# Optimization experiments

Measured on AMD Instinct MI355X. Metric: run time of the kernel, lower is better.

## Reference

```python
import jax, jax.numpy as jnp
import numpy as np

ATTEN_SIZE = 16
HIDDEN = 512


def setup_inputs() -> dict:
    key = jax.random.key(0)
    ks = jax.random.split(key, 6)
    B, S, D_in, H, D_out = 64, 100, 256, HIDDEN, 256
    # xavier-normal-ish scale for weights
    def xav(k, shape):
        fan_in, fan_out = shape
        std = np.sqrt(2.0 / (fan_in + fan_out))
        return jax.random.normal(k, shape, dtype=jnp.float32) * std
    return {
        "x": jax.random.normal(ks[0], (B, S, D_in), dtype=jnp.float32),
        "W0": xav(ks[1], (D_in, H)),
        "b0": jnp.zeros((1, 1, H), dtype=jnp.float32),
        "Wq": xav(ks[2], (H, H)),
        "Wk": xav(ks[3], (H, H)),
        "Wv": xav(ks[4], (H, H)),
        "W1": xav(ks[5], (H, D_out)),
        "b1": jnp.zeros((1, 1, D_out), dtype=jnp.float32),
    }


def reference(x, W0, b0, Wq, Wk, Wv, W1, b1):
    w = ATTEN_SIZE
    win = 2 * w + 1
    B, S = x.shape[0], x.shape[1]
    # pre-attention MLP layer (atten_layer_index = 1)
    h = jax.nn.relu(x @ W0 + b0)  # [B, S, H]
    # sliding-window neighbor gather, matching pad + roll(k) + stack + slice:
    # x_nei[:, i, k_idx] = padded[:, i + 2w - k_idx]  (reversed window order)
    padded = jnp.pad(h, ((0, 0), (w, w), (0, 0)))  # [B, S+2w, H]
    idx = jnp.arange(S)[:, None] + (2 * w - jnp.arange(win))[None, :]
    x_nei = padded[:, idx]
    q = x_nei @ Wq
    k = x_nei @ Wk
    v = x_nei @ Wv
    d = jnp.einsum('bswh,buh_->bswu'.replace('h_', 'sh'[1] + 'h'), q, k) if False else jnp.einsum('bswh,bsuh->bswu', q, k)
    d = d / jnp.sqrt(jnp.float32(HIDDEN))
    alpha = jax.nn.softmax(d, axis=-1)
    wv = jnp.einsum('bswu,bsuh->bswh', alpha, v)
    out = wv.sum(axis=2)  # sum over window rows -> [B, S, H]
    y = jax.nn.relu(out @ W1 + b1)  # [B, S, D_out]
    return y, alpha.reshape(B * S, win, win)
```

## Files before the change

### kernel.cpp

```cpp
#include <hip/hip_runtime.h>

typedef __bf16 bf16x8 __attribute__((ext_vector_type(8)));
typedef float f32x4 __attribute__((ext_vector_type(4)));

__device__ __forceinline__ unsigned short f2bf(float f) {
  unsigned int u = __float_as_uint(f);
  u += 0x7FFFu + ((u >> 16) & 1u);
  return (unsigned short)(u >> 16);
}
__device__ __forceinline__ float bf2f(unsigned short s) {
  return __uint_as_float(((unsigned int)s) << 16);
}

__global__ __launch_bounds__(256) void prep_kernel(
    const float* __restrict__ x, const float* __restrict__ W0,
    const float* __restrict__ Wq, const float* __restrict__ Wk,
    const float* __restrict__ Wv, const float* __restrict__ W1,
    unsigned short* __restrict__ xb, unsigned short* __restrict__ w0t,
    unsigned short* __restrict__ wqkvt, unsigned short* __restrict__ w1t)
{
  int idx = blockIdx.x * 256 + threadIdx.x;
  const int XB = 6400 * 256, W0T = 512 * 256, WQKV = 1536 * 512, W1T = 256 * 512;
  if (idx < XB) { xb[idx] = f2bf(x[idx]); return; }
  idx -= XB;
  if (idx < W0T) {
    int n = idx >> 8, k = idx & 255;
    w0t[idx] = f2bf(W0[k * 512 + n]); return;
  }
  idx -= W0T;
  if (idx < WQKV) {
    int n = idx >> 9, k = idx & 511;
    float v = (n < 512) ? Wq[k * 512 + n]
            : (n < 1024) ? Wk[k * 512 + (n - 512)]
                         : Wv[k * 512 + (n - 1024)];
    wqkvt[idx] = f2bf(v); return;
  }
  idx -= WQKV;
  if (idx < W1T) {
    int n = idx >> 9, k = idx & 511;
    w1t[idx] = f2bf(W1[k * 256 + n]);
  }
}

template<bool RELU, bool OUT_BF16>
__global__ __launch_bounds__(64) void gemm_mfma(
    const unsigned short* __restrict__ A, int lda,
    const unsigned short* __restrict__ Bt, int ldb,
    const float* __restrict__ bias,
    void* __restrict__ Cout, int ldc, int K)
{
  const int m0 = blockIdx.x * 64;
  const int n0 = blockIdx.y * 64;
  const int l  = threadIdx.x;
  const int lr = l & 15;
  const int kq = l >> 4;
  f32x4 acc[4][4];
#pragma unroll
  for (int i = 0; i < 4; i++)
#pragma unroll
    for (int j = 0; j < 4; j++) acc[i][j] = (f32x4){0.f, 0.f, 0.f, 0.f};

  const unsigned short* Ap = A  + (long)(m0 + lr) * lda + 8 * kq;
  const unsigned short* Bp = Bt + (long)(n0 + lr) * ldb + 8 * kq;

  for (int k0 = 0; k0 < K; k0 += 32) {
    bf16x8 af[4], bfr[4];
#pragma unroll
    for (int i = 0; i < 4; i++)
      af[i] = *(const bf16x8*)(Ap + (long)(16 * i) * lda + k0);
#pragma unroll
    for (int j = 0; j < 4; j++)
      bfr[j] = *(const bf16x8*)(Bp + (long)(16 * j) * ldb + k0);
#pragma unroll
    for (int i = 0; i < 4; i++)
#pragma unroll
      for (int j = 0; j < 4; j++)
        acc[i][j] = __builtin_amdgcn_mfma_f32_16x16x32_bf16(af[i], bfr[j], acc[i][j], 0, 0, 0);
  }

#pragma unroll
  for (int i = 0; i < 4; i++) {
#pragma unroll
    for (int j = 0; j < 4; j++) {
      int col = n0 + 16 * j + lr;
      float bv = bias ? bias[col] : 0.0f;
#pragma unroll
      for (int r = 0; r < 4; r++) {
        int row = m0 + 16 * i + 4 * kq + r;
        float v = acc[i][j][r] + bv;
        if (RELU) v = fmaxf(v, 0.0f);
        if (OUT_BF16) ((unsigned short*)Cout)[(long)row * ldc + col] = f2bf(v);
        else          ((float*)Cout)[(long)row * ldc + col] = v;
      }
    }
  }
}

__global__ __launch_bounds__(64) void gram_kernel(
    const unsigned short* __restrict__ qkv, float* __restrict__ G)
{
  const float scale = 0.044194173824159216f;
  const int it = blockIdx.x;
  const int b  = blockIdx.y;
  const int l = threadIdx.x, lr = l & 15, kq = l >> 4;
  const unsigned short* qrow = qkv + (long)(b * 100 + it * 16 + lr) * 1536 + 8 * kq;
  const unsigned short* krow = qkv + (long)(b * 100 + lr) * 1536 + 512 + 8 * kq;
  f32x4 acc[7];
#pragma unroll
  for (int j = 0; j < 7; j++) acc[j] = (f32x4){0.f, 0.f, 0.f, 0.f};
  for (int k0 = 0; k0 < 512; k0 += 32) {
    bf16x8 aq = *(const bf16x8*)(qrow + k0);
#pragma unroll
    for (int j = 0; j < 7; j++) {
      bf16x8 bk = *(const bf16x8*)(krow + (long)(j * 16) * 1536 + k0);
      acc[j] = __builtin_amdgcn_mfma_f32_16x16x32_bf16(aq, bk, acc[j], 0, 0, 0);
    }
  }
  float* Gb = G + (long)b * 10000;
#pragma unroll
  for (int j = 0; j < 7; j++) {
#pragma unroll
    for (int r = 0; r < 4; r++) {
      int i  = it * 16 + 4 * kq + r;
      int jj = j * 16 + lr;
      if (i < 100 && jj < 100) Gb[i * 100 + jj] = acc[j][r] * scale;
    }
  }
}

__global__ __launch_bounds__(256) void attn_kernel(
    const float* __restrict__ G,
    const unsigned short* __restrict__ qkv,
    float* __restrict__ alpha_out,
    unsigned short* __restrict__ outb)
{
  const int blk = blockIdx.x;
  const int b = blk / 100, s = blk % 100;
  __shared__ float dmat[33][36];
  __shared__ float rowmax[33], rowinv[33];
  __shared__ float beta[36];
  const int tid = threadIdx.x;
  const float* Gb = G + (long)b * 10000;

  for (int t = tid; t < 1089; t += 256) {
    int dw = t / 33, du = t % 33;
    int i = s + 16 - dw, j = s + 16 - du;
    float v = 0.f;
    if ((unsigned)i < 100u && (unsigned)j < 100u) v = Gb[i * 100 + j];
    dmat[dw][du] = v;
  }
  __syncthreads();

  if (tid < 132) {
    int row = tid >> 2, g = tid & 3;
    float m = -1e30f;
    for (int u = g; u < 33; u += 4) m = fmaxf(m, dmat[row][u]);
    m = fmaxf(m, __shfl_xor(m, 1));
    m = fmaxf(m, __shfl_xor(m, 2));
    float ssum = 0.f;
    for (int u = g; u < 33; u += 4) ssum += __expf(dmat[row][u] - m);
    ssum += __shfl_xor(ssum, 1);
    ssum += __shfl_xor(ssum, 2);
    if (g == 0) { rowmax[row] = m; rowinv[row] = 1.0f / ssum; }
  }
  __syncthreads();

  float* aout = alpha_out + (long)blk * 1089;
  for (int t = tid; t < 1089; t += 256) {
    int dw = t / 33, du = t % 33;
    float a = __expf(dmat[dw][du] - rowmax[dw]) * rowinv[dw];
    aout[t] = a;
    dmat[dw][du] = a;
  }
  __syncthreads();

  if (tid < 33) {
    float sum = 0.f;
    for (int w = 0; w < 33; ++w) sum += dmat[w][tid];
    beta[tid] = sum;
  }
  __syncthreads();

  const unsigned short* vbase = qkv + (long)(b * 100) * 1536 + 1024;
  {
    int c = tid;
    float acc0 = 0.f, acc1 = 0.f;
    for (int u = 0; u < 33; ++u) {
      int p = s + 16 - u;
      if ((unsigned)p < 100u) {
        float bw = beta[u];
        const unsigned short* vr = vbase + (long)p * 1536;
        acc0 += bw * bf2f(vr[c]);
        acc1 += bw * bf2f(vr[c + 256]);
      }
    }
    unsigned short* orow = outb + (long)blk * 512;
    orow[c]       = f2bf(acc0);
    orow[c + 256] = f2bf(acc1);
  }
}

extern "C" void kernel_launch(void* const* d_in, const int* in_sizes, int n_in,
                              void* d_out, int out_size, void* d_ws, size_t ws_size,
                              hipStream_t stream) {
  const float* x  = (const float*)d_in[0];
  const float* W0 = (const float*)d_in[1];
  const float* b0 = (const float*)d_in[2];
  const float* Wq = (const float*)d_in[3];
  const float* Wk = (const float*)d_in[4];
  const float* Wv = (const float*)d_in[5];
  const float* W1 = (const float*)d_in[6];
  const float* b1 = (const float*)d_in[7];

  char* ws = (char*)d_ws;
  unsigned short* xb    = (unsigned short*)(ws + 0);
  unsigned short* w0t   = (unsigned short*)(ws + 3276800);
  unsigned short* wqkvt = (unsigned short*)(ws + 3538944);
  unsigned short* w1t   = (unsigned short*)(ws + 5111808);
  unsigned short* h     = (unsigned short*)(ws + 5373952);
  unsigned short* qkv   = (unsigned short*)(ws + 11927552);
  float*          G     = (float*)(ws + 31637504);
  unsigned short* outb  = (unsigned short*)(ws + 34197504);

  float* y_out     = (float*)d_out;
  float* alpha_out = y_out + 6400 * 256;

  prep_kernel<<<10496, 256, 0, stream>>>(x, W0, Wq, Wk, Wv, W1, xb, w0t, wqkvt, w1t);
  gemm_mfma<true,  true ><<<dim3(100, 8),  64, 0, stream>>>(xb, 256, w0t, 256, b0, h, 512, 256);
  gemm_mfma<false, true ><<<dim3(100, 24), 64, 0, stream>>>(h, 512, wqkvt, 512, nullptr, qkv, 1536, 512);
  gram_kernel<<<dim3(7, 64), 64, 0, stream>>>(qkv, G);
  attn_kernel<<<6400, 256, 0, stream>>>(G, qkv, alpha_out, outb);
  gemm_mfma<true,  false><<<dim3(100, 4), 64, 0, stream>>>(outb, 512, w1t, 512, b1, y_out, 256, 512);
}
```

Before: 211.3 us.

## Stage GEMM tiles in LDS with async double-buffered loads; tile weight transposes

Replaces the single-wave GEMM and gram kernels, which loaded operands straight from global memory, with 256-thread blocks. These stage 64x32 A and 128x32 B tiles into LDS through global_load_lds and double-buffer them, so loading the next K-slice overlaps the MFMAs on the current one and the tiles are shared across four waves. The prep kernel now converts x with float4 loads and transposes the weights through a padded shared-memory tile, so both reads and writes are coalesced. Gram now reads 128 K rows where 100 are valid, so it computes extra padded work. Workspace offsets shift to make room for that overread.

```diff
diff --git a/kernel.cpp b/kernel.cpp
--- a/kernel.cpp
+++ b/kernel.cpp
@@ -2,6 +2,7 @@
 
 typedef __bf16 bf16x8 __attribute__((ext_vector_type(8)));
 typedef float f32x4 __attribute__((ext_vector_type(4)));
+typedef unsigned int u32;
 
 __device__ __forceinline__ unsigned short f2bf(float f) {
   unsigned int u = __float_as_uint(f);
@@ -10,6 +11,12 @@
 }
 __device__ __forceinline__ float bf2f(unsigned short s) {
   return __uint_as_float(((unsigned int)s) << 16);
+}
+
+__device__ __forceinline__ void gload16(const void* g, void* l) {
+  __builtin_amdgcn_global_load_lds(
+      (const __attribute__((address_space(1))) u32*)g,
+      (__attribute__((address_space(3))) u32*)l, 16, 0, 0);
 }
 
 __global__ __launch_bounds__(256) void prep_kernel(
@@ -19,75 +26,108 @@
     unsigned short* __restrict__ xb, unsigned short* __restrict__ w0t,
     unsigned short* __restrict__ wqkvt, unsigned short* __restrict__ w1t)
 {
-  int idx = blockIdx.x * 256 + threadIdx.x;
-  const int XB = 6400 * 256, W0T = 512 * 256, WQKV = 1536 * 512, W1T = 256 * 512;
-  if (idx < XB) { xb[idx] = f2bf(x[idx]); return; }
-  idx -= XB;
-  if (idx < W0T) {
-    int n = idx >> 8, k = idx & 255;
-    w0t[idx] = f2bf(W0[k * 512 + n]); return;
-  }
-  idx -= W0T;
-  if (idx < WQKV) {
-    int n = idx >> 9, k = idx & 511;
-    float v = (n < 512) ? Wq[k * 512 + n]
-            : (n < 1024) ? Wk[k * 512 + (n - 512)]
-                         : Wv[k * 512 + (n - 1024)];
-    wqkvt[idx] = f2bf(v); return;
-  }
-  idx -= WQKV;
-  if (idx < W1T) {
-    int n = idx >> 9, k = idx & 511;
-    w1t[idx] = f2bf(W1[k * 256 + n]);
+  __shared__ float tile[32][33];
+  const int bid = blockIdx.x, tid = threadIdx.x;
+  if (bid < 1600) {
+    long i = (long)bid * 1024 + tid * 4;
+    float4 v = *(const float4*)(x + i);
+    unsigned short o0 = f2bf(v.x), o1 = f2bf(v.y), o2 = f2bf(v.z), o3 = f2bf(v.w);
+    ushort4 o = {o0, o1, o2, o3};
+    *(ushort4*)(xb + i) = o;
+    return;
+  }
+  int id = bid - 1600;
+  const float* src; unsigned short* dst;
+  int N, DLD, k0, n0, drow0;
+  if (id < 128) {
+    src = W0; N = 512; dst = w0t; DLD = 256;
+    k0 = (id >> 4) * 32; n0 = (id & 15) * 32; drow0 = n0;
+  } else if (id < 896) {
+    int id1 = id - 128, which = id1 >> 8, rem = id1 & 255;
+    src = (which == 0) ? Wq : (which == 1) ? Wk : Wv;
+    N = 512; dst = wqkvt; DLD = 512;
+    k0 = (rem >> 4) * 32; n0 = (rem & 15) * 32; drow0 = which * 512 + n0;
+  } else {
+    int id2 = id - 896;
+    src = W1; N = 256; dst = w1t; DLD = 512;
+    k0 = (id2 >> 3) * 32; n0 = (id2 & 7) * 32; drow0 = n0;
+  }
+  const int tr = tid >> 5, tc = tid & 31;
+#pragma unroll
+  for (int rr = 0; rr < 4; ++rr) {
+    int kl = tr + rr * 8;
+    tile[kl][tc] = src[(long)(k0 + kl) * N + n0 + tc];
+  }
+  __syncthreads();
+#pragma unroll
+  for (int rr = 0; rr < 4; ++rr) {
+    int nl = tr + rr * 8;
+    dst[(long)(drow0 + nl) * DLD + k0 + tc] = f2bf(tile[tc][nl]);
   }
 }
 
 template<bool RELU, bool OUT_BF16>
-__global__ __launch_bounds__(64) void gemm_mfma(
+__global__ __launch_bounds__(256) void gemm_tile(
     const unsigned short* __restrict__ A, int lda,
     const unsigned short* __restrict__ Bt, int ldb,
     const float* __restrict__ bias,
-    void* __restrict__ Cout, int ldc, int K)
+    void* __restrict__ Cout, int ldc, int KT)
 {
+  __shared__ unsigned short As[2][64 * 32];
+  __shared__ unsigned short Bs[2][128 * 32];
+  const int tid = threadIdx.x;
   const int m0 = blockIdx.x * 64;
-  const int n0 = blockIdx.y * 64;
-  const int l  = threadIdx.x;
-  const int lr = l & 15;
-  const int kq = l >> 4;
-  f32x4 acc[4][4];
+  const int n0 = blockIdx.y * 128;
+  const int w = tid >> 6, lane = tid & 63;
+  const int lr = lane & 15, kq = lane >> 4;
+
+  const unsigned short* Ag  = A  + (long)(m0 + (tid >> 2)) * lda + (tid & 3) * 8;
+  const unsigned short* Bg0 = Bt + (long)(n0 + (tid >> 2)) * ldb + (tid & 3) * 8;
+  const unsigned short* Bg1 = Bg0 + (long)64 * ldb;
+
+  f32x4 acc[4][2];
 #pragma unroll
   for (int i = 0; i < 4; i++)
 #pragma unroll
-    for (int j = 0; j < 4; j++) acc[i][j] = (f32x4){0.f, 0.f, 0.f, 0.f};
-
-  const unsigned short* Ap = A  + (long)(m0 + lr) * lda + 8 * kq;
-  const unsigned short* Bp = Bt + (long)(n0 + lr) * ldb + 8 * kq;
-
-  for (int k0 = 0; k0 < K; k0 += 32) {
-    bf16x8 af[4], bfr[4];
-#pragma unroll
-    for (int i = 0; i < 4; i++)
-      af[i] = *(const bf16x8*)(Ap + (long)(16 * i) * lda + k0);
-#pragma unroll
-    for (int j = 0; j < 4; j++)
-      bfr[j] = *(const bf16x8*)(Bp + (long)(16 * j) * ldb + k0);
-#pragma unroll
-    for (int i = 0; i < 4; i++)
-#pragma unroll
-      for (int j = 0; j < 4; j++)
-        acc[i][j] = __builtin_amdgcn_mfma_f32_16x16x32_bf16(af[i], bfr[j], acc[i][j], 0, 0, 0);
-  }
-
-#pragma unroll
-  for (int i = 0; i < 4; i++) {
-#pragma unroll
-    for (int j = 0; j < 4; j++) {
-      int col = n0 + 16 * j + lr;
+    for (int j = 0; j < 2; j++) acc[i][j] = (f32x4){0.f, 0.f, 0.f, 0.f};
+
+#define STAGE(buf, kt) do { int ko = (kt) * 32;                      \
+    gload16(Ag + ko,  &As[buf][tid * 8]);                            \
+    gload16(Bg0 + ko, &Bs[buf][tid * 8]);                            \
+    gload16(Bg1 + ko, &Bs[buf][(tid + 256) * 8]); } while (0)
+
+  STAGE(0, 0);
+  __syncthreads();
+  int cur = 0;
+  for (int kt = 0; kt < KT; ++kt) {
+    if (kt + 1 < KT) STAGE(cur ^ 1, kt + 1);
+    bf16x8 af[4], bfr[2];
+#pragma unroll
+    for (int ii = 0; ii < 4; ii++)
+      af[ii] = *(const bf16x8*)&As[cur][(16 * ii + lr) * 32 + 8 * kq];
+#pragma unroll
+    for (int jj = 0; jj < 2; jj++)
+      bfr[jj] = *(const bf16x8*)&Bs[cur][(w * 32 + 16 * jj + lr) * 32 + 8 * kq];
+#pragma unroll
+    for (int ii = 0; ii < 4; ii++)
+#pragma unroll
+      for (int jj = 0; jj < 2; jj++)
+        acc[ii][jj] = __builtin_amdgcn_mfma_f32_16x16x32_bf16(af[ii], bfr[jj], acc[ii][jj], 0, 0, 0);
+    __syncthreads();
+    cur ^= 1;
+  }
+#undef STAGE
+
+#pragma unroll
+  for (int ii = 0; ii < 4; ii++) {
+#pragma unroll
+    for (int jj = 0; jj < 2; jj++) {
+      int col = n0 + w * 32 + 16 * jj + lr;
       float bv = bias ? bias[col] : 0.0f;
 #pragma unroll
       for (int r = 0; r < 4; r++) {
-        int row = m0 + 16 * i + 4 * kq + r;
-        float v = acc[i][j][r] + bv;
+        int row = m0 + 16 * ii + 4 * kq + r;
+        float v = acc[ii][jj][r] + bv;
         if (RELU) v = fmaxf(v, 0.0f);
         if (OUT_BF16) ((unsigned short*)Cout)[(long)row * ldc + col] = f2bf(v);
         else          ((float*)Cout)[(long)row * ldc + col] = v;
@@ -96,34 +136,68 @@
   }
 }
 
-__global__ __launch_bounds__(64) void gram_kernel(
+__global__ __launch_bounds__(256) void gram_tile(
     const unsigned short* __restrict__ qkv, float* __restrict__ G)
 {
   const float scale = 0.044194173824159216f;
-  const int it = blockIdx.x;
+  __shared__ unsigned short As[2][64 * 32];
+  __shared__ unsigned short Bs[2][128 * 32];
+  const int tid = threadIdx.x;
+  const int m0 = blockIdx.x * 64;
   const int b  = blockIdx.y;
-  const int l = threadIdx.x, lr = l & 15, kq = l >> 4;
-  const unsigned short* qrow = qkv + (long)(b * 100 + it * 16 + lr) * 1536 + 8 * kq;
-  const unsigned short* krow = qkv + (long)(b * 100 + lr) * 1536 + 512 + 8 * kq;
-  f32x4 acc[7];
-#pragma unroll
-  for (int j = 0; j < 7; j++) acc[j] = (f32x4){0.f, 0.f, 0.f, 0.f};
-  for (int k0 = 0; k0 < 512; k0 += 32) {
-    bf16x8 aq = *(const bf16x8*)(qrow + k0);
-#pragma unroll
-    for (int j = 0; j < 7; j++) {
-      bf16x8 bk = *(const bf16x8*)(krow + (long)(j * 16) * 1536 + k0);
-      acc[j] = __builtin_amdgcn_mfma_f32_16x16x32_bf16(aq, bk, acc[j], 0, 0, 0);
-    }
-  }
+  const int w = tid >> 6, lane = tid & 63;
+  const int lr = lane & 15, kq = lane >> 4;
+
+  const unsigned short* A  = qkv + (long)b * 100 * 1536;
+  const unsigned short* Bt = A + 512;
+  const unsigned short* Ag  = A  + (long)(m0 + (tid >> 2)) * 1536 + (tid & 3) * 8;
+  const unsigned short* Bg0 = Bt + (long)(tid >> 2) * 1536 + (tid & 3) * 8;
+  const unsigned short* Bg1 = Bg0 + (long)64 * 1536;
+
+  f32x4 acc[4][2];
+#pragma unroll
+  for (int i = 0; i < 4; i++)
+#pragma unroll
+    for (int j = 0; j < 2; j++) acc[i][j] = (f32x4){0.f, 0.f, 0.f, 0.f};
+
+#define STAGE(buf, kt) do { int ko = (kt) * 32;                      \
+    gload16(Ag + ko,  &As[buf][tid * 8]);                            \
+    gload16(Bg0 + ko, &Bs[buf][tid * 8]);                            \
+    gload16(Bg1 + ko, &Bs[buf][(tid + 256) * 8]); } while (0)
+
+  STAGE(0, 0);
+  __syncthreads();
+  int cur = 0;
+  for (int kt = 0; kt < 16; ++kt) {
+    if (kt + 1 < 16) STAGE(cur ^ 1, kt + 1);
+    bf16x8 af[4], bfr[2];
+#pragma unroll
+    for (int ii = 0; ii < 4; ii++)
+      af[ii] = *(const bf16x8*)&As[cur][(16 * ii + lr) * 32 + 8 * kq];
+#pragma unroll
+    for (int jj = 0; jj < 2; jj++)
+      bfr[jj] = *(const bf16x8*)&Bs[cur][(w * 32 + 16 * jj + lr) * 32 + 8 * kq];
+#pragma unroll
+    for (int ii = 0; ii < 4; ii++)
+#pragma unroll
+      for (int jj = 0; jj < 2; jj++)
+        acc[ii][jj] = __builtin_amdgcn_mfma_f32_16x16x32_bf16(af[ii], bfr[jj], acc[ii][jj], 0, 0, 0);
+    __syncthreads();
+    cur ^= 1;
+  }
+#undef STAGE
+
   float* Gb = G + (long)b * 10000;
 #pragma unroll
-  for (int j = 0; j < 7; j++) {
-#pragma unroll
-    for (int r = 0; r < 4; r++) {
-      int i  = it * 16 + 4 * kq + r;
-      int jj = j * 16 + lr;
-      if (i < 100 && jj < 100) Gb[i * 100 + jj] = acc[j][r] * scale;
+  for (int ii = 0; ii < 4; ii++) {
+#pragma unroll
+    for (int jj = 0; jj < 2; jj++) {
+      int j = w * 32 + 16 * jj + lr;
+#pragma unroll
+      for (int r = 0; r < 4; r++) {
+        int i = m0 + 16 * ii + 4 * kq + r;
+        if (i < 100 && j < 100) Gb[i * 100 + j] = acc[ii][jj][r] * scale;
+      }
     }
   }
 }
@@ -219,16 +293,16 @@
   unsigned short* w1t   = (unsigned short*)(ws + 5111808);
   unsigned short* h     = (unsigned short*)(ws + 5373952);
   unsigned short* qkv   = (unsigned short*)(ws + 11927552);
-  float*          G     = (float*)(ws + 31637504);
-  unsigned short* outb  = (unsigned short*)(ws + 34197504);
+  float*          G     = (float*)(ws + 31686656);
+  unsigned short* outb  = (unsigned short*)(ws + 34246656);
 
   float* y_out     = (float*)d_out;
   float* alpha_out = y_out + 6400 * 256;
 
-  prep_kernel<<<10496, 256, 0, stream>>>(x, W0, Wq, Wk, Wv, W1, xb, w0t, wqkvt, w1t);
-  gemm_mfma<true,  true ><<<dim3(100, 8),  64, 0, stream>>>(xb, 256, w0t, 256, b0, h, 512, 256);
-  gemm_mfma<false, true ><<<dim3(100, 24), 64, 0, stream>>>(h, 512, wqkvt, 512, nullptr, qkv, 1536, 512);
-  gram_kernel<<<dim3(7, 64), 64, 0, stream>>>(qkv, G);
+  prep_kernel<<<2624, 256, 0, stream>>>(x, W0, Wq, Wk, Wv, W1, xb, w0t, wqkvt, w1t);
+  gemm_tile<true,  true ><<<dim3(100, 4),  256, 0, stream>>>(xb, 256, w0t, 256, b0, h, 512, 8);
+  gemm_tile<false, true ><<<dim3(100, 12), 256, 0, stream>>>(h, 512, wqkvt, 512, nullptr, qkv, 1536, 16);
+  gram_tile<<<dim3(2, 64), 256, 0, stream>>>(qkv, G);
   attn_kernel<<<6400, 256, 0, stream>>>(G, qkv, alpha_out, outb);
-  gemm_mfma<true,  false><<<dim3(100, 4), 64, 0, stream>>>(outb, 512, w1t, 512, b1, y_out, 256, 512);
-}
+  gemm_tile<true,  false><<<dim3(100, 2),  256, 0, stream>>>(outb, 512, w1t, 512, b1, y_out, 256, 16);
+}
```

Result: faster. 178.2 us (-15.6%).
